# Kernel optimization log

Hardware: AMD Instinct MI355X
Metric: run time of the kernel (lower is better)

The kernel has to match this reference:

```python
import jax, jax.numpy as jnp
import numpy as np
import math

B, T, L = 32, 512, 128
IN_C, D, H, NL = 512, 512, 8, 6
HD = D // H
DFF = 2 * D  # dim_feedforward = hidden_dim * 2 per __init__
V = 8000
BASE = 10000.0
EPS = 1e-5


def _rope_tables(n, hd):
    # standard RoPE: half-dim frequencies duplicated, matching precompute_rope_sin_cos
    inv = 1.0 / (BASE ** (jnp.arange(0, hd, 2, dtype=jnp.float32) / hd))
    ang = jnp.arange(n, dtype=jnp.float32)[:, None] * inv[None, :]  # [n, hd/2]
    cos = jnp.concatenate([jnp.cos(ang), jnp.cos(ang)], axis=-1)    # [n, hd]
    sin = jnp.concatenate([jnp.sin(ang), jnp.sin(ang)], axis=-1)
    return cos, sin


def _rot_half(x):
    x1, x2 = jnp.split(x, 2, axis=-1)
    return jnp.concatenate([-x2, x1], axis=-1)


def _ln(x, g, b):
    m = x.mean(-1, keepdims=True)
    v = jnp.mean((x - m) ** 2, axis=-1, keepdims=True)
    return (x - m) / jnp.sqrt(v + EPS) * g + b


def setup_inputs() -> dict:
    key = jax.random.key(0)
    ks = jax.random.split(key, 24)
    w = lambda k, s: jax.random.normal(k, s, jnp.float32) * 0.02
    z = lambda s: jnp.zeros(s, jnp.float32)
    o = lambda s: jnp.ones(s, jnp.float32)
    return {
        'encoder_features': jax.random.normal(ks[0], (B, T, IN_C), jnp.float32),
        'targets': jax.random.randint(ks[1], (B, L), 0, V),
        'emb': w(ks[2], (V, D)),
        'inp_w': w(ks[3], (D, IN_C)), 'inp_b': z((D,)),
        'out_w': w(ks[4], (V, D)), 'out_b': z((V,)),
        'qw': w(ks[5], (D, D)), 'qb': z((D,)),
        'kw': w(ks[6], (D, D)), 'kb': z((D,)),
        'vw': w(ks[7], (D, D)), 'vb': z((D,)),
        'ow': w(ks[8], (D, D)), 'ob': z((D,)),
        'mha_w': w(ks[9], (3 * D, D)), 'mha_b': z((3 * D,)),
        'mha_ow': w(ks[10], (D, D)), 'mha_ob': z((D,)),
        'w1': w(ks[11], (DFF, D)), 'b1': z((DFF,)),
        'w2': w(ks[12], (D, DFF)), 'b2': z((D,)),
        'ln1_g': o((D,)), 'ln1_b': z((D,)),
        'ln2_g': o((D,)), 'ln2_b': z((D,)),
        'ln3_g': o((D,)), 'ln3_b': z((D,)),
    }


def reference(encoder_features, targets, emb, inp_w, inp_b, out_w, out_b,
              qw, qb, kw, kb, vw, vb, ow, ob, mha_w, mha_b, mha_ow, mha_ob,
              w1, b1, w2, b2, ln1_g, ln1_b, ln2_g, ln2_b, ln3_g, ln3_b):
    memory = encoder_features @ inp_w.T + inp_b               # [B,T,D]
    tgt = emb[targets] * math.sqrt(D)                          # [B,L,D]
    mem_pad = jnp.abs(memory).sum(-1) == 0                     # [B,T] key padding mask
    causal = jnp.tril(jnp.ones((L, L), dtype=bool))
    cos, sin = _rope_tables(L, HD)                             # pos_ids = arange(0, L)
    scale = 1.0 / math.sqrt(HD)
    wq, wk, wv = jnp.split(mha_w, 3, axis=0)
    bq, bk, bv = jnp.split(mha_b, 3)

    for _ in range(NL):  # all layers share the same weights (ModuleList of one object)
        # --- self-attention with RoPE ---
        q = (tgt @ qw.T + qb).reshape(B, L, H, HD).transpose(0, 2, 1, 3)
        k = (tgt @ kw.T + kb).reshape(B, L, H, HD).transpose(0, 2, 1, 3)
        v = (tgt @ vw.T + vb).reshape(B, L, H, HD).transpose(0, 2, 1, 3)
        q = q * cos + _rot_half(q) * sin
        k = k * cos + _rot_half(k) * sin
        s = jnp.einsum('bhqd,bhkd->bhqk', q, k) * scale
        s = jnp.where(causal, s, -jnp.inf)
        a = jax.nn.softmax(s, axis=-1)
        o_sa = jnp.einsum('bhqk,bhkd->bhqd', a, v).transpose(0, 2, 1, 3).reshape(B, L, D)
        tgt = _ln(tgt + o_sa @ ow.T + ob, ln1_g, ln1_b)
        # --- cross-attention (nn.MultiheadAttention, batch_first) ---
        q2 = (tgt @ wq.T + bq).reshape(B, L, H, HD).transpose(0, 2, 1, 3)
        k2 = (memory @ wk.T + bk).reshape(B, T, H, HD).transpose(0, 2, 1, 3)
        v2 = (memory @ wv.T + bv).reshape(B, T, H, HD).transpose(0, 2, 1, 3)
        s2 = jnp.einsum('bhqd,bhkd->bhqk', q2, k2) * scale
        s2 = jnp.where(mem_pad[:, None, None, :], -jnp.inf, s2)
        a2 = jax.nn.softmax(s2, axis=-1)
        o_ca = jnp.einsum('bhqk,bhkd->bhqd', a2, v2).transpose(0, 2, 1, 3).reshape(B, L, D)
        tgt = _ln(tgt + o_ca @ mha_ow.T + mha_ob, ln2_g, ln2_b)
        # --- FFN (exact GELU, as nn.GELU default) ---
        ff = jax.nn.gelu(tgt @ w1.T + b1, approximate=False) @ w2.T + b2
        tgt = _ln(tgt + ff, ln3_g, ln3_b)

    logits = tgt @ out_w.T + out_b  # [B,L,V]
    return logits, tgt
```

## Files before the change

### kernel.cpp

```cpp
#include <hip/hip_runtime.h>
#include <hip/hip_bf16.h>

#define B_ 32
#define T_ 512
#define L_ 128
#define INC_ 512
#define D_ 512
#define H_ 8
#define HD_ 64
#define NL_ 6
#define DFF_ 1024
#define V_ 8000
#define LDSK 40
#define AST 72

typedef __bf16 bfr;
typedef __attribute__((ext_vector_type(8))) __bf16 bf16x8;
typedef __attribute__((ext_vector_type(4))) __bf16 bf16x4;
typedef __attribute__((ext_vector_type(4))) float f32x4;

struct ConvDesc { const float* src; bfr* dst; int n; int blk0; };
struct ConvTable { ConvDesc e[12]; int ne; };

__global__ void conv_many_kernel(ConvTable tab)
{
    int b = blockIdx.x;
    for (int i = 0; i < tab.ne; ++i) {
        const ConvDesc d = tab.e[i];
        int nb = (d.n + 255) >> 8;
        if (b >= d.blk0 && b < d.blk0 + nb) {
            int g = (b - d.blk0) * 256 + threadIdx.x;
            if (g < d.n) d.dst[g] = (bfr)d.src[g];
            return;
        }
    }
}

__device__ __forceinline__ void tile_map(int bid, int nbm, int nbn, int& pm, int& pn)
{
    int nwg = nbm * nbn;
    int q = nwg >> 3, r = nwg & 7;
    int xcd = bid & 7, idx = bid >> 3;
    int wgid = (xcd < r ? xcd * (q + 1) : r * (q + 1) + (xcd - r) * q) + idx;
    const int GROUP = 8;
    int per_group = GROUP * nbn;
    int gid = wgid / per_group;
    int first = gid * GROUP;
    int gsz = min(nbm - first, GROUP);
    int rem = wgid - gid * per_group;
    pm = first + rem % gsz;
    pn = rem / gsz;
}

template <int OUT>
__global__ __launch_bounds__(256) void gemm_split(
    const float* __restrict__ A, const bfr* __restrict__ Whi,
    const float* __restrict__ bias, float* __restrict__ Cf, bfr* __restrict__ Cb,
    int M, int N, int K)
{
    __shared__ bfr Ah_s[128 * LDSK];
    __shared__ bfr Wh_s[64 * LDSK];
    const int t = threadIdx.x;
    const int bm = blockIdx.y * 128, bn = blockIdx.x * 64;
    const int w = t >> 6, lane = t & 63;
    const int wm = w >> 1, wn = w & 1;
    const int fr = lane & 15, kq = lane >> 4;
    const int ar = t >> 1, ah = (t & 1) * 16;
    const int wr = t >> 2, wk = (t & 3) * 8;

    f32x4 acc[4][2] = {};

    for (int k0 = 0; k0 < K; k0 += 32) {
        {
            const float* ap = A + (size_t)(bm + ar) * K + (k0 + ah);
            float4 v0 = ((const float4*)ap)[0];
            float4 v1 = ((const float4*)ap)[1];
            float4 v2 = ((const float4*)ap)[2];
            float4 v3 = ((const float4*)ap)[3];
            float xs[16] = {v0.x, v0.y, v0.z, v0.w, v1.x, v1.y, v1.z, v1.w,
                            v2.x, v2.y, v2.z, v2.w, v3.x, v3.y, v3.z, v3.w};
            bf16x8 h0, h1;
#pragma unroll
            for (int i = 0; i < 8; ++i) h0[i] = (bfr)xs[i];
#pragma unroll
            for (int i = 0; i < 8; ++i) h1[i] = (bfr)xs[8 + i];
            *(bf16x8*)(Ah_s + ar * LDSK + ah) = h0;
            *(bf16x8*)(Ah_s + ar * LDSK + ah + 8) = h1;
        }
        *(bf16x8*)(Wh_s + wr * LDSK + wk) = *(const bf16x8*)(Whi + (size_t)(bn + wr) * K + (k0 + wk));
        __syncthreads();
        bf16x8 Afh[4], Wfh[2];
#pragma unroll
        for (int i = 0; i < 4; ++i)
            Afh[i] = *(const bf16x8*)(Ah_s + (wm * 64 + i * 16 + fr) * LDSK + kq * 8);
#pragma unroll
        for (int j = 0; j < 2; ++j)
            Wfh[j] = *(const bf16x8*)(Wh_s + (wn * 32 + j * 16 + fr) * LDSK + kq * 8);
#pragma unroll
        for (int i = 0; i < 4; ++i)
#pragma unroll
            for (int j = 0; j < 2; ++j)
                acc[i][j] = __builtin_amdgcn_mfma_f32_16x16x32_bf16(Afh[i], Wfh[j], acc[i][j], 0, 0, 0);
        __syncthreads();
    }
#pragma unroll
    for (int i = 0; i < 4; ++i) {
        int row0 = bm + wm * 64 + i * 16 + (lane >> 4) * 4;
#pragma unroll
        for (int j = 0; j < 2; ++j) {
            int col = bn + wn * 32 + j * 16 + fr;
            float bj = bias[col];
#pragma unroll
            for (int r = 0; r < 4; ++r) {
                float v = acc[i][j][r] + bj;
                if (OUT == 0) Cf[(size_t)(row0 + r) * N + col] = v;
                else Cb[(size_t)(row0 + r) * N + col] = (bfr)v;
            }
        }
    }
}

template <int ACT, int OUT, int BM>
__global__ __launch_bounds__(256, 2) void gemm_ps(
    const bfr* __restrict__ Ahi,
    const bfr* __restrict__ Whi,
    const float* __restrict__ bias, float* __restrict__ Cf,
    bfr* __restrict__ Chi, int M, int N, int K)
{
    constexpr int MF = BM / 32;
    __shared__ bfr Ah_s[BM * LDSK];
    __shared__ bfr Wh_s[64 * LDSK];
    const int t = threadIdx.x;
    int pm, pn;
    tile_map(blockIdx.x, M / BM, N / 64, pm, pn);
    const int bm = pm * BM, bn = pn * 64;
    const int w = t >> 6, lane = t & 63;
    const int wm = w >> 1, wn = w & 1;
    const int fr = lane & 15, kq = lane >> 4;
    const int wr = t >> 2, wk = (t & 3) * 8;

    f32x4 acc[MF][2] = {};

    for (int k0 = 0; k0 < K; k0 += 32) {
        if constexpr (BM == 128) {
            const int ar = t >> 1, ah = (t & 1) * 16;
            const bfr* ap = Ahi + (size_t)(bm + ar) * K + (k0 + ah);
            *(bf16x8*)(Ah_s + ar * LDSK + ah) = *(const bf16x8*)ap;
            *(bf16x8*)(Ah_s + ar * LDSK + ah + 8) = *(const bf16x8*)(ap + 8);
        } else {
            const int ar = t >> 2, ah = (t & 3) * 8;
            *(bf16x8*)(Ah_s + ar * LDSK + ah) = *(const bf16x8*)(Ahi + (size_t)(bm + ar) * K + (k0 + ah));
        }
        *(bf16x8*)(Wh_s + wr * LDSK + wk) = *(const bf16x8*)(Whi + (size_t)(bn + wr) * K + (k0 + wk));
        __syncthreads();
        bf16x8 Afh[MF], Wfh[2];
#pragma unroll
        for (int i = 0; i < MF; ++i)
            Afh[i] = *(const bf16x8*)(Ah_s + (wm * (BM / 2) + i * 16 + fr) * LDSK + kq * 8);
#pragma unroll
        for (int j = 0; j < 2; ++j)
            Wfh[j] = *(const bf16x8*)(Wh_s + (wn * 32 + j * 16 + fr) * LDSK + kq * 8);
#pragma unroll
        for (int i = 0; i < MF; ++i)
#pragma unroll
            for (int j = 0; j < 2; ++j)
                acc[i][j] = __builtin_amdgcn_mfma_f32_16x16x32_bf16(Afh[i], Wfh[j], acc[i][j], 0, 0, 0);
        __syncthreads();
    }
#pragma unroll
    for (int i = 0; i < MF; ++i) {
        int row0 = bm + wm * (BM / 2) + i * 16 + (lane >> 4) * 4;
#pragma unroll
        for (int j = 0; j < 2; ++j) {
            int col = bn + wn * 32 + j * 16 + fr;
            float bj = bias[col];
#pragma unroll
            for (int r = 0; r < 4; ++r) {
                float v = acc[i][j][r] + bj;
                if (ACT == 1) v = 0.5f * v * (1.0f + erff(v * 0.70710678118654752f));
                size_t idx = (size_t)(row0 + r) * N + col;
                if (OUT == 0) Cf[idx] = v;
                else Chi[idx] = (bfr)v;
            }
        }
    }
}

template <int TK, int CAUSAL>
__global__ __launch_bounds__(256) void attn_kernel(
    const bfr* __restrict__ Qg, int qstr,
    const bfr* __restrict__ Kg, const bfr* __restrict__ Vg, int kvstr,
    const int* __restrict__ pad,
    const float* __restrict__ cosT, const float* __restrict__ sinT,
    bfr* __restrict__ Ohi)
{
    __shared__ bfr Qs[64 * AST];
    __shared__ bfr Ks[64 * AST];
    __shared__ bfr VTs[64 * AST];
    __shared__ bfr Ps[64 * AST];
    const int bidx = blockIdx.x;
    const int qt = bidx & 1, bh = bidx >> 1;
    const int h = bh & 7, b = bh >> 3;
    const int t = threadIdx.x;
    const int w = t >> 6, lane = t & 63;
    const int l4 = lane & 15, hi4 = lane >> 4;
    const int q0 = qt * 64;
    const int srow = t >> 2, ht = t & 3;

    if (CAUSAL) {
        int qrow = q0 + srow;
        const bfr* qp = Qg + (size_t)(b * L_ + qrow) * qstr + h * HD_ + ht * 8;
        bf16x8 a = *(const bf16x8*)qp;
        bf16x8 bb = *(const bf16x8*)(qp + 32);
        bf16x8 o1, o2;
#pragma unroll
        for (int j = 0; j < 8; ++j) {
            float c = cosT[qrow * 32 + ht * 8 + j], s = sinT[qrow * 32 + ht * 8 + j];
            float x1 = (float)a[j], x2 = (float)bb[j];
            o1[j] = (bfr)(x1 * c - x2 * s);
            o2[j] = (bfr)(x2 * c + x1 * s);
        }
        *(bf16x8*)(Qs + srow * AST + ht * 8) = o1;
        *(bf16x8*)(Qs + srow * AST + ht * 8 + 32) = o2;
    } else {
        const bfr* qp = Qg + (size_t)(b * L_ + q0 + srow) * qstr + h * HD_ + ht * 16;
        *(bf16x8*)(Qs + srow * AST + ht * 16) = *(const bf16x8*)qp;
        *(bf16x8*)(Qs + srow * AST + ht * 16 + 8) = *(const bf16x8*)(qp + 8);
    }

    f32x4 o_acc[4] = {};
    float m_run[4], l_run[4];
#pragma unroll
    for (int r = 0; r < 4; ++r) { m_run[r] = -1e30f; l_run[r] = 0.f; }

    const int NT = CAUSAL ? (qt + 1) : (TK / 64);
    for (int kt = 0; kt < NT; ++kt) {
        __syncthreads();
        if (CAUSAL) {
            int krow = kt * 64 + srow;
            const bfr* kp = Kg + (size_t)(b * TK + krow) * kvstr + h * HD_ + ht * 8;
            bf16x8 a = *(const bf16x8*)kp;
            bf16x8 bb = *(const bf16x8*)(kp + 32);
            bf16x8 o1, o2;
#pragma unroll
            for (int j = 0; j < 8; ++j) {
                float c = cosT[krow * 32 + ht * 8 + j], s = sinT[krow * 32 + ht * 8 + j];
                float x1 = (float)a[j], x2 = (float)bb[j];
                o1[j] = (bfr)(x1 * c - x2 * s);
                o2[j] = (bfr)(x2 * c + x1 * s);
            }
            *(bf16x8*)(Ks + srow * AST + ht * 8) = o1;
            *(bf16x8*)(Ks + srow * AST + ht * 8 + 32) = o2;
        } else {
            const bfr* kp = Kg + (size_t)(b * TK + kt * 64 + srow) * kvstr + h * HD_ + ht * 16;
            *(bf16x8*)(Ks + srow * AST + ht * 16) = *(const bf16x8*)kp;
            *(bf16x8*)(Ks + srow * AST + ht * 16 + 8) = *(const bf16x8*)(kp + 8);
        }
        {
            const bfr* vp = Vg + (size_t)(b * TK + kt * 64 + srow) * kvstr + h * HD_ + ht * 16;
            bf16x8 v0 = *(const bf16x8*)vp;
            bf16x8 v1 = *(const bf16x8*)(vp + 8);
#pragma unroll
            for (int i = 0; i < 8; ++i) VTs[(ht * 16 + i) * AST + srow] = v0[i];
#pragma unroll
            for (int i = 0; i < 8; ++i) VTs[(ht * 16 + 8 + i) * AST + srow] = v1[i];
        }
        __syncthreads();

        f32x4 s[4] = {};
#pragma unroll
        for (int kk = 0; kk < 64; kk += 32) {
            bf16x8 a = *(const bf16x8*)(Qs + (w * 16 + l4) * AST + kk + hi4 * 8);
#pragma unroll
            for (int n = 0; n < 4; ++n) {
                bf16x8 bb = *(const bf16x8*)(Ks + (n * 16 + l4) * AST + kk + hi4 * 8);
                s[n] = __builtin_amdgcn_mfma_f32_16x16x32_bf16(a, bb, s[n], 0, 0, 0);
            }
        }
        float madd[4];
        if (!CAUSAL) {
#pragma unroll
            for (int n = 0; n < 4; ++n)
                madd[n] = pad[b * TK + kt * 64 + n * 16 + l4] ? -1e30f : 0.f;
        }
#pragma unroll
        for (int r = 0; r < 4; ++r) {
            int qrow = q0 + w * 16 + hi4 * 4 + r;
            float sv[4];
#pragma unroll
            for (int n = 0; n < 4; ++n) {
                float x = s[n][r] * 0.125f;
                if (CAUSAL) {
                    int col = kt * 64 + n * 16 + l4;
                    if (col > qrow) x = -1e30f;
                } else x += madd[n];
                sv[n] = x;
            }
            float mx = fmaxf(fmaxf(sv[0], sv[1]), fmaxf(sv[2], sv[3]));
#pragma unroll
            for (int off = 1; off < 16; off <<= 1) mx = fmaxf(mx, __shfl_xor(mx, off));
            float mnew = fmaxf(m_run[r], mx);
            float alpha = expf(m_run[r] - mnew);
            float pv[4], psum = 0.f;
#pragma unroll
            for (int n = 0; n < 4; ++n) { pv[n] = expf(sv[n] - mnew); psum += pv[n]; }
#pragma unroll
            for (int off = 1; off < 16; off <<= 1) psum += __shfl_xor(psum, off);
            l_run[r] = l_run[r] * alpha + psum;
            m_run[r] = mnew;
#pragma unroll
            for (int n = 0; n < 4; ++n) o_acc[n][r] *= alpha;
#pragma unroll
            for (int n = 0; n < 4; ++n)
                Ps[(w * 16 + hi4 * 4 + r) * AST + n * 16 + l4] = (bfr)pv[n];
        }
#pragma unroll
        for (int kk = 0; kk < 64; kk += 32) {
            bf16x8 pa = *(const bf16x8*)(Ps + (w * 16 + l4) * AST + kk + hi4 * 8);
#pragma unroll
            for (int n = 0; n < 4; ++n) {
                bf16x8 vb = *(const bf16x8*)(VTs + (n * 16 + l4) * AST + kk + hi4 * 8);
                o_acc[n] = __builtin_amdgcn_mfma_f32_16x16x32_bf16(pa, vb, o_acc[n], 0, 0, 0);
            }
        }
    }
#pragma unroll
    for (int r = 0; r < 4; ++r) {
        float inv = 1.0f / l_run[r];
        int qrow = q0 + w * 16 + hi4 * 4 + r;
#pragma unroll
        for (int n = 0; n < 4; ++n)
            Ohi[(size_t)(b * L_ + qrow) * D_ + h * HD_ + n * 16 + l4] = (bfr)(o_acc[n][r] * inv);
    }
}

__global__ void rope_tables_kernel(float* __restrict__ cosT, float* __restrict__ sinT)
{
    int gid = blockIdx.x * blockDim.x + threadIdx.x;
    if (gid >= L_ * 32) return;
    int l = gid >> 5, i = gid & 31;
    float inv = powf(10000.0f, -(float)(2 * i) / (float)HD_);
    float ang = (float)l * inv;
    cosT[gid] = cosf(ang);
    sinT[gid] = sinf(ang);
}

__global__ void embed_kernel(const int* __restrict__ targets, const float* __restrict__ emb,
                             float* __restrict__ tgt, bfr* __restrict__ thi)
{
    int gid = blockIdx.x * blockDim.x + threadIdx.x;
    if (gid >= B_ * L_ * D_) return;
    int d = gid & (D_ - 1);
    int r = gid >> 9;
    int tok = targets[r];
    float x = emb[(size_t)tok * D_ + d] * 22.62741699796952f;
    tgt[gid] = x;
    thi[gid] = (bfr)x;
}

__global__ void pad_kernel(const float* __restrict__ mem, int* __restrict__ pad)
{
    int gid = blockIdx.x * blockDim.x + threadIdx.x;
    if (gid >= B_ * T_) return;
    const float* p = mem + (size_t)gid * D_;
    float s = 0.f;
    for (int d = 0; d < D_; ++d) s += fabsf(p[d]);
    pad[gid] = (s == 0.0f) ? 1 : 0;
}

__global__ __launch_bounds__(128) void ln_residual_kernel(
    float* __restrict__ tgt, const float* __restrict__ delta,
    const float* __restrict__ g, const float* __restrict__ bb,
    bfr* __restrict__ thi)
{
    const int row = blockIdx.x;
    const int t = threadIdx.x;
    __shared__ float rbuf[128];
    size_t base = (size_t)row * D_ + t * 4;
    float4 x = *(float4*)(tgt + base);
    float4 dl = *(const float4*)(delta + base);
    x.x += dl.x; x.y += dl.y; x.z += dl.z; x.w += dl.w;
    rbuf[t] = x.x + x.y + x.z + x.w;
    __syncthreads();
    for (int off = 64; off > 0; off >>= 1) { if (t < off) rbuf[t] += rbuf[t + off]; __syncthreads(); }
    float mean = rbuf[0] * (1.0f / D_);
    __syncthreads();
    float4 d4 = {x.x - mean, x.y - mean, x.z - mean, x.w - mean};
    rbuf[t] = d4.x * d4.x + d4.y * d4.y + d4.z * d4.z + d4.w * d4.w;
    __syncthreads();
    for (int off = 64; off > 0; off >>= 1) { if (t < off) rbuf[t] += rbuf[t + off]; __syncthreads(); }
    float inv = 1.0f / sqrtf(rbuf[0] * (1.0f / D_) + 1e-5f);
    float4 g4 = *(const float4*)(g + t * 4);
    float4 b4 = *(const float4*)(bb + t * 4);
    float4 y = {d4.x * inv * g4.x + b4.x, d4.y * inv * g4.y + b4.y,
                d4.z * inv * g4.z + b4.z, d4.w * inv * g4.w + b4.w};
    *(float4*)(tgt + base) = y;
    bf16x4 h4 = {(bfr)y.x, (bfr)y.y, (bfr)y.z, (bfr)y.w};
    *(bf16x4*)(thi + base) = h4;
}

__global__ void copyf_kernel(const float* __restrict__ in, float* __restrict__ out, int n)
{
    int gid = blockIdx.x * blockDim.x + threadIdx.x;
    if (gid < n) out[gid] = in[gid];
}

__global__ void fillf_kernel(float* p, float v, size_t n)
{
    size_t gid = (size_t)blockIdx.x * 256 + threadIdx.x;
    if (gid < n) p[gid] = v;
}

extern "C" void kernel_launch(void* const* d_in, const int* in_sizes, int n_in,
                              void* d_out, int out_size, void* d_ws, size_t ws_size,
                              hipStream_t stream)
{
    const float* enc    = (const float*)d_in[0];
    const int*   tg     = (const int*)d_in[1];
    const float* emb    = (const float*)d_in[2];
    const float* inp_w  = (const float*)d_in[3];
    const float* inp_b  = (const float*)d_in[4];
    const float* out_w  = (const float*)d_in[5];
    const float* out_b  = (const float*)d_in[6];
    const float* qw     = (const float*)d_in[7];
    const float* qb     = (const float*)d_in[8];
    const float* kw     = (const float*)d_in[9];
    const float* kb     = (const float*)d_in[10];
    const float* vw     = (const float*)d_in[11];
    const float* vb     = (const float*)d_in[12];
    const float* ow     = (const float*)d_in[13];
    const float* ob     = (const float*)d_in[14];
    const float* mha_w  = (const float*)d_in[15];
    const float* mha_b  = (const float*)d_in[16];
    const float* mha_ow = (const float*)d_in[17];
    const float* mha_ob = (const float*)d_in[18];
    const float* w1     = (const float*)d_in[19];
    const float* b1     = (const float*)d_in[20];
    const float* w2     = (const float*)d_in[21];
    const float* b2     = (const float*)d_in[22];
    const float* ln1g   = (const float*)d_in[23];
    const float* ln1b   = (const float*)d_in[24];
    const float* ln2g   = (const float*)d_in[25];
    const float* ln2b   = (const float*)d_in[26];
    const float* ln3g   = (const float*)d_in[27];
    const float* ln3b   = (const float*)d_in[28];

    const int BL = B_ * L_;
    const int BT = B_ * T_;
    const size_t N_LOGITS = (size_t)BL * V_;
    const int D2 = D_ * D_;

    const size_t WS_NEEDED =
        (size_t)BT * 1024 * sizeof(bfr)
        + (size_t)BL * D_ * sizeof(float)
        + (size_t)BL * D_ * sizeof(bfr)
        + (size_t)2 * L_ * 32 * sizeof(float) + (size_t)BT * sizeof(int)
        + (size_t)V_ * D_ * sizeof(bfr);
    if (ws_size < WS_NEEDED) {
        fillf_kernel<<<((size_t)out_size + 255) / 256, 256, 0, stream>>>((float*)d_out, 0.f, (size_t)out_size);
        return;
    }
    bfr*   f_KVb = (bfr*)d_ws;
    float* f_tgt = (float*)(f_KVb + (size_t)BT * 1024);
    bfr*   tgt_hi = (bfr*)(f_tgt + (size_t)BL * D_);
    float* f_cos = (float*)(tgt_hi + (size_t)BL * D_);
    float* f_sin = f_cos + (size_t)L_ * 32;
    int*   f_pad = (int*)(f_sin + (size_t)L_ * 32);
    bfr*   ow_hi = (bfr*)(f_pad + BT);

    bfr* wp = (bfr*)d_out;
    bfr* qkvw_hi = wp;  wp += 3 * D2;
    bfr* inp_hi  = wp;  wp += D2;
    bfr* mha_hi  = wp;  wp += 3 * D2;
    bfr* o_hi    = wp;  wp += D2;
    bfr* mo_hi   = wp;  wp += D2;
    bfr* w1_hi   = wp;  wp += DFF_ * D_;
    bfr* w2_hi   = wp;  wp += D_ * DFF_;
    float* f_qkvb = (float*)wp;
    float* lr    = f_qkvb + 3 * D_;
    float* f_t2  = lr;
    bfr*   qkv   = (bfr*)(f_t2 + (size_t)BL * D_);
    bfr*   qcr   = qkv + (size_t)BL * 3 * D_;
    bfr*   t1_hi = qcr + (size_t)BL * D_;
    bfr*   ffh_hi = t1_hi + (size_t)BL * D_;
    float* f_mem = lr;

    {
        ConvTable tab{};
        int blk = 0, ne = 0;
        auto add = [&](const float* s, bfr* d, int n) {
            tab.e[ne] = {s, d, n, blk};
            blk += (n + 255) >> 8;
            ++ne;
        };
        add(qw, qkvw_hi, D2);
        add(kw, qkvw_hi + D2, D2);
        add(vw, qkvw_hi + 2 * D2, D2);
        add(inp_w, inp_hi, D2);
        add(mha_w, mha_hi, 3 * D2);
        add(ow, o_hi, D2);
        add(mha_ow, mo_hi, D2);
        add(w1, w1_hi, DFF_ * D_);
        add(w2, w2_hi, D_ * DFF_);
        add(out_w, ow_hi, V_ * D_);
        tab.ne = ne;
        conv_many_kernel<<<blk, 256, 0, stream>>>(tab);
    }
    copyf_kernel<<<2, 256, 0, stream>>>(qb, f_qkvb, D_);
    copyf_kernel<<<2, 256, 0, stream>>>(kb, f_qkvb + D_, D_);
    copyf_kernel<<<2, 256, 0, stream>>>(vb, f_qkvb + 2 * D_, D_);

    rope_tables_kernel<<<(L_ * 32 + 255) / 256, 256, 0, stream>>>(f_cos, f_sin);
    embed_kernel<<<(BL * D_ + 255) / 256, 256, 0, stream>>>(tg, emb, f_tgt, tgt_hi);

    gemm_split<0><<<dim3(D_ / 64, BT / 128), 256, 0, stream>>>(enc, inp_hi, inp_b, f_mem, nullptr, BT, D_, INC_);
    pad_kernel<<<(BT + 255) / 256, 256, 0, stream>>>(f_mem, f_pad);
    gemm_split<1><<<dim3(1024 / 64, BT / 128), 256, 0, stream>>>(f_mem, mha_hi + (size_t)D2, mha_b + D_, nullptr, f_KVb, BT, 1024, D_);

    for (int layer = 0; layer < NL_; ++layer) {
        gemm_ps<0, 1, 64><<<(BL / 64) * (3 * D_ / 64), 256, 0, stream>>>(tgt_hi, qkvw_hi, f_qkvb, nullptr, qkv, BL, 3 * D_, D_);
        attn_kernel<L_, 1><<<B_ * H_ * 2, 256, 0, stream>>>(qkv, 3 * D_, qkv + D_, qkv + 2 * D_, 3 * D_, nullptr, f_cos, f_sin, t1_hi);
        gemm_ps<0, 0, 64><<<(BL / 64) * (D_ / 64), 256, 0, stream>>>(t1_hi, o_hi, ob, f_t2, nullptr, BL, D_, D_);
        ln_residual_kernel<<<BL, 128, 0, stream>>>(f_tgt, f_t2, ln1g, ln1b, tgt_hi);
        gemm_ps<0, 1, 64><<<(BL / 64) * (D_ / 64), 256, 0, stream>>>(tgt_hi, mha_hi, mha_b, nullptr, qcr, BL, D_, D_);
        attn_kernel<T_, 0><<<B_ * H_ * 2, 256, 0, stream>>>(qcr, D_, f_KVb, f_KVb + D_, 1024, f_pad, nullptr, nullptr, t1_hi);
        gemm_ps<0, 0, 64><<<(BL / 64) * (D_ / 64), 256, 0, stream>>>(t1_hi, mo_hi, mha_ob, f_t2, nullptr, BL, D_, D_);
        ln_residual_kernel<<<BL, 128, 0, stream>>>(f_tgt, f_t2, ln2g, ln2b, tgt_hi);
        gemm_ps<1, 1, 64><<<(BL / 64) * (DFF_ / 64), 256, 0, stream>>>(tgt_hi, w1_hi, b1, nullptr, ffh_hi, BL, DFF_, D_);
        gemm_ps<0, 0, 64><<<(BL / 64) * (D_ / 64), 256, 0, stream>>>(ffh_hi, w2_hi, b2, f_t2, nullptr, BL, D_, DFF_);
        ln_residual_kernel<<<BL, 128, 0, stream>>>(f_tgt, f_t2, ln3g, ln3b, tgt_hi);
    }

    float* o_logits = (float*)d_out;
    float* o_tgt = o_logits + N_LOGITS;
    gemm_ps<0, 0, 128><<<(BL / 128) * (V_ / 64), 256, 0, stream>>>(tgt_hi, ow_hi, out_b, o_logits, nullptr, BL, V_, D_);
    copyf_kernel<<<(BL * D_ + 255) / 256, 256, 0, stream>>>(f_tgt, o_tgt, BL * D_);
}
```

Measured before the change: 1.107 ms.

## Fuse output projections with residual add and LayerNorm in one GEMM kernel

Adds a gemm_ln kernel where each block computes a full 32x512 output row tile, then applies bias, the residual add and LayerNorm in registers using shuffle and shared-memory reductions. It replaces the three projection GEMM + ln_residual pairs per layer, removing the fp32 intermediate round-trip and half of those launches. The trade-offs are only 128 blocks of large tiles (lower parallelism, heavy register use), a single-pass variance formula, and f_mem moved to a new workspace slot.

```diff
diff --git a/kernel.cpp b/kernel.cpp
--- a/kernel.cpp
+++ b/kernel.cpp
@@ -186,6 +186,99 @@
     }
 }
 
+__global__ __launch_bounds__(256, 2) void gemm_ln(
+    const bfr* __restrict__ Ahi, const bfr* __restrict__ Whi,
+    const float* __restrict__ bias,
+    float* __restrict__ resid, const float* __restrict__ g, const float* __restrict__ bb,
+    bfr* __restrict__ thi, int K)
+{
+    __shared__ bfr A_s[32 * LDSK];
+    __shared__ bfr W_s[512 * LDSK];
+    __shared__ float redS[32][2];
+    __shared__ float redQ[32][2];
+    const int t = threadIdx.x;
+    const int w = t >> 6, lane = t & 63;
+    const int s = w >> 1, c = w & 1;
+    const int fr = lane & 15, kq = lane >> 4;
+    const int bm = blockIdx.x * 32;
+
+    f32x4 acc[16] = {};
+
+    for (int k0 = 0; k0 < K; k0 += 32) {
+        {
+            const int ar = t >> 3, ah = (t & 7) * 4;
+            *(bf16x4*)(A_s + ar * LDSK + ah) = *(const bf16x4*)(Ahi + (size_t)(bm + ar) * K + (k0 + ah));
+        }
+        {
+            const int wr = t * 2;
+            const bfr* wp = Whi + (size_t)wr * K + k0;
+#pragma unroll
+            for (int q = 0; q < 4; ++q)
+                *(bf16x8*)(W_s + wr * LDSK + q * 8) = *(const bf16x8*)(wp + q * 8);
+            wp += K;
+#pragma unroll
+            for (int q = 0; q < 4; ++q)
+                *(bf16x8*)(W_s + (wr + 1) * LDSK + q * 8) = *(const bf16x8*)(wp + q * 8);
+        }
+        __syncthreads();
+        bf16x8 Af = *(const bf16x8*)(A_s + (s * 16 + fr) * LDSK + kq * 8);
+#pragma unroll
+        for (int j = 0; j < 16; ++j) {
+            bf16x8 Wf = *(const bf16x8*)(W_s + (c * 256 + j * 16 + fr) * LDSK + kq * 8);
+            acc[j] = __builtin_amdgcn_mfma_f32_16x16x32_bf16(Af, Wf, acc[j], 0, 0, 0);
+        }
+        __syncthreads();
+    }
+
+    float sum[4] = {}, sq[4] = {};
+#pragma unroll
+    for (int j = 0; j < 16; ++j) {
+        int col = c * 256 + j * 16 + fr;
+        float bj = bias[col];
+#pragma unroll
+        for (int r = 0; r < 4; ++r) {
+            int row = bm + s * 16 + kq * 4 + r;
+            float x = acc[j][r] + bj + resid[(size_t)row * D_ + col];
+            acc[j][r] = x;
+            sum[r] += x;
+            sq[r] += x * x;
+        }
+    }
+#pragma unroll
+    for (int off = 1; off < 16; off <<= 1) {
+#pragma unroll
+        for (int r = 0; r < 4; ++r) {
+            sum[r] += __shfl_xor(sum[r], off);
+            sq[r] += __shfl_xor(sq[r], off);
+        }
+    }
+    if (fr == 0) {
+#pragma unroll
+        for (int r = 0; r < 4; ++r) {
+            redS[s * 16 + kq * 4 + r][c] = sum[r];
+            redQ[s * 16 + kq * 4 + r][c] = sq[r];
+        }
+    }
+    __syncthreads();
+#pragma unroll
+    for (int r = 0; r < 4; ++r) {
+        int ri = s * 16 + kq * 4 + r;
+        float S = redS[ri][0] + redS[ri][1];
+        float Q = redQ[ri][0] + redQ[ri][1];
+        float mean = S * (1.0f / D_);
+        float var = Q * (1.0f / D_) - mean * mean;
+        float inv = 1.0f / sqrtf(var + 1e-5f);
+        int row = bm + ri;
+#pragma unroll
+        for (int j = 0; j < 16; ++j) {
+            int col = c * 256 + j * 16 + fr;
+            float y = (acc[j][r] - mean) * inv * g[col] + bb[col];
+            resid[(size_t)row * D_ + col] = y;
+            thi[(size_t)row * D_ + col] = (bfr)y;
+        }
+    }
+}
+
 template <int TK, int CAUSAL>
 __global__ __launch_bounds__(256) void attn_kernel(
     const bfr* __restrict__ Qg, int qstr,
@@ -366,37 +459,6 @@
     float s = 0.f;
     for (int d = 0; d < D_; ++d) s += fabsf(p[d]);
     pad[gid] = (s == 0.0f) ? 1 : 0;
-}
-
-__global__ __launch_bounds__(128) void ln_residual_kernel(
-    float* __restrict__ tgt, const float* __restrict__ delta,
-    const float* __restrict__ g, const float* __restrict__ bb,
-    bfr* __restrict__ thi)
-{
-    const int row = blockIdx.x;
-    const int t = threadIdx.x;
-    __shared__ float rbuf[128];
-    size_t base = (size_t)row * D_ + t * 4;
-    float4 x = *(float4*)(tgt + base);
-    float4 dl = *(const float4*)(delta + base);
-    x.x += dl.x; x.y += dl.y; x.z += dl.z; x.w += dl.w;
-    rbuf[t] = x.x + x.y + x.z + x.w;
-    __syncthreads();
-    for (int off = 64; off > 0; off >>= 1) { if (t < off) rbuf[t] += rbuf[t + off]; __syncthreads(); }
-    float mean = rbuf[0] * (1.0f / D_);
-    __syncthreads();
-    float4 d4 = {x.x - mean, x.y - mean, x.z - mean, x.w - mean};
-    rbuf[t] = d4.x * d4.x + d4.y * d4.y + d4.z * d4.z + d4.w * d4.w;
-    __syncthreads();
-    for (int off = 64; off > 0; off >>= 1) { if (t < off) rbuf[t] += rbuf[t + off]; __syncthreads(); }
-    float inv = 1.0f / sqrtf(rbuf[0] * (1.0f / D_) + 1e-5f);
-    float4 g4 = *(const float4*)(g + t * 4);
-    float4 b4 = *(const float4*)(bb + t * 4);
-    float4 y = {d4.x * inv * g4.x + b4.x, d4.y * inv * g4.y + b4.y,
-                d4.z * inv * g4.z + b4.z, d4.w * inv * g4.w + b4.w};
-    *(float4*)(tgt + base) = y;
-    bf16x4 h4 = {(bfr)y.x, (bfr)y.y, (bfr)y.z, (bfr)y.w};
-    *(bf16x4*)(thi + base) = h4;
 }
 
 __global__ void copyf_kernel(const float* __restrict__ in, float* __restrict__ out, int n)
@@ -478,12 +540,12 @@
     bfr* w2_hi   = wp;  wp += D_ * DFF_;
     float* f_qkvb = (float*)wp;
     float* lr    = f_qkvb + 3 * D_;
-    float* f_t2  = lr;
-    bfr*   qkv   = (bfr*)(f_t2 + (size_t)BL * D_);
+    bfr*   qkv   = (bfr*)lr;
     bfr*   qcr   = qkv + (size_t)BL * 3 * D_;
     bfr*   t1_hi = qcr + (size_t)BL * D_;
     bfr*   ffh_hi = t1_hi + (size_t)BL * D_;
     float* f_mem = lr;
+    float* f_mem2 = (float*)(ffh_hi + (size_t)BL * DFF_);
 
     {
         ConvTable tab{};
@@ -513,22 +575,19 @@
     rope_tables_kernel<<<(L_ * 32 + 255) / 256, 256, 0, stream>>>(f_cos, f_sin);
     embed_kernel<<<(BL * D_ + 255) / 256, 256, 0, stream>>>(tg, emb, f_tgt, tgt_hi);
 
-    gemm_split<0><<<dim3(D_ / 64, BT / 128), 256, 0, stream>>>(enc, inp_hi, inp_b, f_mem, nullptr, BT, D_, INC_);
-    pad_kernel<<<(BT + 255) / 256, 256, 0, stream>>>(f_mem, f_pad);
-    gemm_split<1><<<dim3(1024 / 64, BT / 128), 256, 0, stream>>>(f_mem, mha_hi + (size_t)D2, mha_b + D_, nullptr, f_KVb, BT, 1024, D_);
+    gemm_split<0><<<dim3(D_ / 64, BT / 128), 256, 0, stream>>>(enc, inp_hi, inp_b, f_mem2, nullptr, BT, D_, INC_);
+    pad_kernel<<<(BT + 255) / 256, 256, 0, stream>>>(f_mem2, f_pad);
+    gemm_split<1><<<dim3(1024 / 64, BT / 128), 256, 0, stream>>>(f_mem2, mha_hi + (size_t)D2, mha_b + D_, nullptr, f_KVb, BT, 1024, D_);
 
     for (int layer = 0; layer < NL_; ++layer) {
         gemm_ps<0, 1, 64><<<(BL / 64) * (3 * D_ / 64), 256, 0, stream>>>(tgt_hi, qkvw_hi, f_qkvb, nullptr, qkv, BL, 3 * D_, D_);
         attn_kernel<L_, 1><<<B_ * H_ * 2, 256, 0, stream>>>(qkv, 3 * D_, qkv + D_, qkv + 2 * D_, 3 * D_, nullptr, f_cos, f_sin, t1_hi);
-        gemm_ps<0, 0, 64><<<(BL / 64) * (D_ / 64), 256, 0, stream>>>(t1_hi, o_hi, ob, f_t2, nullptr, BL, D_, D_);
-        ln_residual_kernel<<<BL, 128, 0, stream>>>(f_tgt, f_t2, ln1g, ln1b, tgt_hi);
+        gemm_ln<<<BL / 32, 256, 0, stream>>>(t1_hi, o_hi, ob, f_tgt, ln1g, ln1b, tgt_hi, D_);
         gemm_ps<0, 1, 64><<<(BL / 64) * (D_ / 64), 256, 0, stream>>>(tgt_hi, mha_hi, mha_b, nullptr, qcr, BL, D_, D_);
         attn_kernel<T_, 0><<<B_ * H_ * 2, 256, 0, stream>>>(qcr, D_, f_KVb, f_KVb + D_, 1024, f_pad, nullptr, nullptr, t1_hi);
-        gemm_ps<0, 0, 64><<<(BL / 64) * (D_ / 64), 256, 0, stream>>>(t1_hi, mo_hi, mha_ob, f_t2, nullptr, BL, D_, D_);
-        ln_residual_kernel<<<BL, 128, 0, stream>>>(f_tgt, f_t2, ln2g, ln2b, tgt_hi);
+        gemm_ln<<<BL / 32, 256, 0, stream>>>(t1_hi, mo_hi, mha_ob, f_tgt, ln2g, ln2b, tgt_hi, D_);
         gemm_ps<1, 1, 64><<<(BL / 64) * (DFF_ / 64), 256, 0, stream>>>(tgt_hi, w1_hi, b1, nullptr, ffh_hi, BL, DFF_, D_);
-        gemm_ps<0, 0, 64><<<(BL / 64) * (D_ / 64), 256, 0, stream>>>(ffh_hi, w2_hi, b2, f_t2, nullptr, BL, D_, DFF_);
-        ln_residual_kernel<<<BL, 128, 0, stream>>>(f_tgt, f_t2, ln3g, ln3b, tgt_hi);
+        gemm_ln<<<BL / 32, 256, 0, stream>>>(ffh_hi, w2_hi, b2, f_tgt, ln3g, ln3b, tgt_hi, DFF_);
     }
 
     float* o_logits = (float*)d_out;
```

Result: slower. 1.507 ms (+36.1%).
